# Performance work log

Hardware: AMD Instinct MI355X
Metric: run time of the kernel (lower is better)

## Reference

```python
import jax, jax.numpy as jnp
import numpy as np

CODEBOOK_SIZE = 1024
CODE_DIM = 64
COMMITMENT_COST = 0.25
EMA_DECAY = 0.99
EPS = 1e-05


def setup_inputs() -> dict:
    key = jax.random.key(0)
    k1, k2, k3, k4 = jax.random.split(key, 4)
    z = jax.random.normal(k1, (16, 4096, CODE_DIM), dtype=jnp.float32)
    codebook = jax.random.normal(k2, (CODEBOOK_SIZE, CODE_DIM), dtype=jnp.float32)
    ema_cluster_size = jax.random.uniform(k3, (CODEBOOK_SIZE,), dtype=jnp.float32)
    ema_w = jax.random.normal(k4, (CODEBOOK_SIZE, CODE_DIM), dtype=jnp.float32)
    return {"z": z, "codebook": codebook, "ema_cluster_size": ema_cluster_size, "ema_w": ema_w}


def reference(z, codebook, ema_cluster_size, ema_w):
    B, T, D = z.shape
    K = CODEBOOK_SIZE
    z_flat = z.reshape(-1, D)  # [N, D]

    # Squared-distance expansion: ||z||^2 + ||c||^2 - 2 z c^T  -> [N, K]
    distances = (
        jnp.sum(z_flat * z_flat, axis=-1, keepdims=True)
        + jnp.sum(codebook * codebook, axis=-1)
        - 2.0 * jnp.matmul(z_flat, codebook.T)
    )
    indices = jnp.argmin(distances, axis=-1)  # [N]
    z_q = codebook[indices]  # [N, D] (gathered from OLD codebook)

    # --- EMA codebook update (training, no_grad in torch) ---
    ones = jnp.ones((z_flat.shape[0],), dtype=z_flat.dtype)
    cluster_size = jax.ops.segment_sum(ones, indices, num_segments=K)  # == one_hot.sum(0)
    cluster_sum = jax.ops.segment_sum(z_flat, indices, num_segments=K)  # == one_hot.T @ z_flat
    new_ecs = ema_cluster_size * EMA_DECAY + (1.0 - EMA_DECAY) * cluster_size
    new_ew = ema_w * EMA_DECAY + (1.0 - EMA_DECAY) * cluster_sum
    n = jnp.sum(new_ecs)
    cluster_size_stable = (new_ecs + EPS) / (n + K * EPS) * n
    new_codebook = new_ew / cluster_size_stable[:, None]

    # Commitment loss (EMA path): commitment_cost * mse(z_flat, stop_grad(z_q))
    commitment_loss = jnp.mean((z_flat - jax.lax.stop_gradient(z_q)) ** 2)
    vq_loss = COMMITMENT_COST * commitment_loss

    # Straight-through estimator
    z_q_st = z_flat + jax.lax.stop_gradient(z_q - z_flat)

    z_q_out = z_q_st.reshape(B, T, D)
    indices_out = indices.reshape(B, T)
    return (z_q_out, vq_loss, indices_out, new_codebook, new_ecs, new_ew)
```

## Files before the change

kernel.cpp:

```cpp
#include <hip/hip_runtime.h>

#define KC   1024
#define DD   64
#define NR   65536

#define DECAY     0.99f
#define ONEM      0.01f
#define EPSV      1e-5f
#define MARGIN_W  0.008f

#define OFF_ZQ    0
#define OFF_LOSS  4194304
#define OFF_IDX   4194305
#define OFF_NCB   4259841
#define OFF_NECS  4325377
#define OFF_NEW   4326401


typedef float  f32x4   __attribute__((ext_vector_type(4)));
typedef short  bf16x8  __attribute__((ext_vector_type(8)));

__device__ __forceinline__ unsigned short b16(float v) {
    union { float f; unsigned u; } x; x.f = v;
    return (unsigned short)((x.u + 0x7fffu + ((x.u >> 16) & 1u)) >> 16);
}
__device__ __forceinline__ float b2f(unsigned short h) {
    union { unsigned u; float f; } x; x.u = (unsigned)h << 16;
    return x.f;
}

__device__ __forceinline__ void gload_lds16(const void* g, void* l) {
    __builtin_amdgcn_global_load_lds(
        (const __attribute__((address_space(1))) unsigned int*)g,
        (__attribute__((address_space(3))) unsigned int*)l, 16, 0, 0);
}

__global__ void vq_prep(const float* __restrict__ cb, float* __restrict__ out,
                        unsigned short* __restrict__ cbh,
                        unsigned short* __restrict__ cbm,
                        float* __restrict__ cbT) {
    const int tid = blockIdx.x * blockDim.x + threadIdx.x;
    if (tid < 65536) {
        const int code = tid >> 6, d = tid & 63;
        const int h2   = code >> 9;
        const int loc  = code & 511;
        const int ch   = loc >> 5;
        const int gloc = loc & 31;
        const int grp  = gloc >> 4;
        const int col  = gloc & 15;
        const int kh   = d >> 5;
        const int hi2  = (d >> 3) & 3;
        const int e    = d & 7;
        const int pi   = ch * 4096 + h2 * 2048 + (grp * 2 + kh) * 512
                       + (hi2 * 16 + col) * 8 + e;
        const float v = cb[tid];
        const unsigned short h = b16(v);
        cbh[pi] = h;
        cbm[pi] = b16(v - b2f(h));
        cbT[d * 1024 + code] = v;
    }
    if (tid < 1024) {
        const float4* c = reinterpret_cast<const float4*>(cb + tid * 64);
        float s = 0.f;
        #pragma unroll
        for (int j = 0; j < 16; ++j) {
            const float4 v = c[j];
            s += v.x*v.x + v.y*v.y + v.z*v.z + v.w*v.w;
        }
        out[OFF_NCB + tid] = s;
    }
    if (tid == 0) out[OFF_LOSS] = 0.0f;
}

__global__ __launch_bounds__(512, 2) void vq_main(const float* __restrict__ z,
                                                  const float* __restrict__ cc,
                                                  const unsigned short* __restrict__ cbh,
                                                  const unsigned short* __restrict__ cbm,
                                                  const float* __restrict__ cbT,
                                                  const float* __restrict__ cb,
                                                  unsigned short* __restrict__ idxw,
                                                  float* __restrict__ out) {
    const int t    = threadIdx.x;
    const int lane = t & 63;
    const int wid  = t >> 6;
    const int rowgrp = wid & 3;
    const int hf     = wid >> 2;
    const int rowbase = blockIdx.x * 128;

    __shared__ char  ldsB[4][16384];
    __shared__ float s_cc[1024];
    __shared__ float s_hd[2][128];
    __shared__ int   s_hi[2][128];
    __shared__ float s_h2[2][128];
    __shared__ int   s_final[128];
    __shared__ int   s_flag[128];
    __shared__ float s_cd[8][32];
    __shared__ int   s_cix[8][32];
    __shared__ float s_red[8];
    __shared__ int   s_nflag;

    if (t == 0) s_nflag = 0;
    s_cc[t]       = cc[t];
    s_cc[t + 512] = cc[t + 512];

    #pragma unroll
    for (int c0 = 0; c0 < 2; ++c0) {
        const char* sh = (const char*)cbh + c0 * 8192 + wid * 1024 + lane * 16;
        const char* sm = (const char*)cbm + c0 * 8192 + wid * 1024 + lane * 16;
        gload_lds16(sh, &ldsB[c0][wid * 1024]);
        gload_lds16(sm, &ldsB[c0][8192 + wid * 1024]);
    }

    bf16x8 a0h[2], a0m[2], a1h[2], a1m[2];
    #pragma unroll
    for (int tile = 0; tile < 2; ++tile) {
        const int ar = rowbase + rowgrp * 32 + tile * 16 + (lane & 15);
        const int kb = (lane >> 4) * 8;
        const float* zr = z + (size_t)ar * 64 + kb;
        const float4 v0a = *reinterpret_cast<const float4*>(zr);
        const float4 v0b = *reinterpret_cast<const float4*>(zr + 4);
        const float4 v1a = *reinterpret_cast<const float4*>(zr + 32);
        const float4 v1b = *reinterpret_cast<const float4*>(zr + 36);
        const float z0[8] = {v0a.x, v0a.y, v0a.z, v0a.w, v0b.x, v0b.y, v0b.z, v0b.w};
        const float z1[8] = {v1a.x, v1a.y, v1a.z, v1a.w, v1b.x, v1b.y, v1b.z, v1b.w};
        #pragma unroll
        for (int e = 0; e < 8; ++e) {
            const unsigned short h0 = b16(z0[e]);
            a0h[tile][e] = (short)h0;
            a0m[tile][e] = (short)b16(z0[e] - b2f(h0));
            const unsigned short h1 = b16(z1[e]);
            a1h[tile][e] = (short)h1;
            a1m[tile][e] = (short)b16(z1[e] - b2f(h1));
        }
    }
    asm volatile("s_waitcnt vmcnt(2)" ::: "memory");
    __builtin_amdgcn_s_barrier();
    __builtin_amdgcn_sched_barrier(0);

    const int lcol   = lane & 15;
    const int lane16 = lane * 16;

    float bd[2][4], b2v[2][4]; int bk[2][4];
    #pragma unroll
    for (int tile = 0; tile < 2; ++tile)
        #pragma unroll
        for (int j = 0; j < 4; ++j) {
            bd[tile][j] = 3.4e38f; b2v[tile][j] = 3.4e38f; bk[tile][j] = 0;
        }

    for (int c = 0; c < 16; ++c) {
        if (c + 2 < 16) {
            const char* sh = (const char*)cbh + (c + 2) * 8192 + wid * 1024 + lane * 16;
            const char* sm = (const char*)cbm + (c + 2) * 8192 + wid * 1024 + lane * 16;
            gload_lds16(sh, &ldsB[(c + 2) & 3][wid * 1024]);
            gload_lds16(sm, &ldsB[(c + 2) & 3][8192 + wid * 1024]);
        }
        const char* bhp = ldsB[c & 3] + hf * 4096;
        const char* bmp = ldsB[c & 3] + 8192 + hf * 4096;

        f32x4 acc00 = {0.f,0.f,0.f,0.f}, acc01 = {0.f,0.f,0.f,0.f};
        f32x4 acc10 = {0.f,0.f,0.f,0.f}, acc11 = {0.f,0.f,0.f,0.f};
        #pragma unroll
        for (int grp = 0; grp < 2; ++grp) {
            #pragma unroll
            for (int kh = 0; kh < 2; ++kh) {
                const bf16x8 bh = *reinterpret_cast<const bf16x8*>(
                    bhp + (grp * 2 + kh) * 1024 + lane16);
                const bf16x8 bm = *reinterpret_cast<const bf16x8*>(
                    bmp + (grp * 2 + kh) * 1024 + lane16);
                const bf16x8 ahh0 = kh ? a1h[0] : a0h[0];
                const bf16x8 amm0 = kh ? a1m[0] : a0m[0];
                const bf16x8 ahh1 = kh ? a1h[1] : a0h[1];
                const bf16x8 amm1 = kh ? a1m[1] : a0m[1];
                f32x4& a0 = grp ? acc01 : acc00;
                f32x4& a1 = grp ? acc11 : acc10;
                a0 = __builtin_amdgcn_mfma_f32_16x16x32_bf16(amm0, bh, a0, 0, 0, 0);
                a1 = __builtin_amdgcn_mfma_f32_16x16x32_bf16(amm1, bh, a1, 0, 0, 0);
                a0 = __builtin_amdgcn_mfma_f32_16x16x32_bf16(ahh0, bm, a0, 0, 0, 0);
                a1 = __builtin_amdgcn_mfma_f32_16x16x32_bf16(ahh1, bm, a1, 0, 0, 0);
                a0 = __builtin_amdgcn_mfma_f32_16x16x32_bf16(ahh0, bh, a0, 0, 0, 0);
                a1 = __builtin_amdgcn_mfma_f32_16x16x32_bf16(ahh1, bh, a1, 0, 0, 0);
            }
        }
        #pragma unroll
        for (int grp = 0; grp < 2; ++grp) {
            const int  code = hf * 512 + c * 32 + grp * 16 + lcol;
            const float ccv = s_cc[code];
            const f32x4 p0 = grp ? acc01 : acc00;
            const f32x4 p1 = grp ? acc11 : acc10;
            #pragma unroll
            for (int j = 0; j < 4; ++j) {
                const float s0 = fmaf(-2.f, p0[j], ccv);
                b2v[0][j] = __builtin_amdgcn_fmed3f(bd[0][j], s0, b2v[0][j]);
                if (s0 < bd[0][j]) { bd[0][j] = s0; bk[0][j] = code; }
                const float s1 = fmaf(-2.f, p1[j], ccv);
                b2v[1][j] = __builtin_amdgcn_fmed3f(bd[1][j], s1, b2v[1][j]);
                if (s1 < bd[1][j]) { bd[1][j] = s1; bk[1][j] = code; }
            }
        }

        if (c < 15) {
            if (c == 14) asm volatile("s_waitcnt vmcnt(0)" ::: "memory");
            else         asm volatile("s_waitcnt vmcnt(2)" ::: "memory");
            __builtin_amdgcn_s_barrier();
            __builtin_amdgcn_sched_barrier(0);
        }
    }

    #pragma unroll
    for (int m = 1; m < 16; m <<= 1) {
        #pragma unroll
        for (int tile = 0; tile < 2; ++tile)
            #pragma unroll
            for (int j = 0; j < 4; ++j) {
                const float od = __shfl_xor(bd[tile][j],  m);
                const int   oi = __shfl_xor(bk[tile][j],  m);
                const float o2 = __shfl_xor(b2v[tile][j], m);
                const float nb2 = fminf(fmaxf(bd[tile][j], od), fminf(b2v[tile][j], o2));
                if (od < bd[tile][j] || (od == bd[tile][j] && oi < bk[tile][j])) {
                    bd[tile][j] = od; bk[tile][j] = oi;
                }
                b2v[tile][j] = nb2;
            }
    }
    if ((lane & 15) == 0) {
        #pragma unroll
        for (int tile = 0; tile < 2; ++tile)
            #pragma unroll
            for (int j = 0; j < 4; ++j) {
                const int r = rowgrp * 32 + tile * 16 + ((lane >> 4) << 2) + j;
                s_hd[hf][r] = bd[tile][j];
                s_hi[hf][r] = bk[tile][j];
                s_h2[hf][r] = b2v[tile][j];
            }
    }
    __syncthreads();

    if (t < 128) {
        const float d0 = s_hd[0][t], d1 = s_hd[1][t];
        float bb = d0; int bi = s_hi[0][t];
        if (d1 < bb) { bb = d1; bi = s_hi[1][t]; }
        const float sec = fminf(fmaxf(d0, d1), fminf(s_h2[0][t], s_h2[1][t]));
        s_final[t] = bi;
        if (sec - bb < MARGIN_W) {
            const int p = atomicAdd(&s_nflag, 1);
            s_flag[p] = t;
        }
    }
    __syncthreads();

    const int nf = s_nflag;
    for (int fb = 0; fb < nf; fb += 32) {
        const int ne = (nf - fb < 32) ? (nf - fb) : 32;
        {
            const int cbase2 = wid * 128;
            const int c0i = cbase2 + lane, c1i = c0i + 64;
            for (int i = 0; i < ne; ++i) {
                const int r = s_flag[fb + i];
                const float* zrow = z + (size_t)(rowbase + r) * 64;
                float a0 = 0.f, a1 = 0.f;
                #pragma unroll 8
                for (int d = 0; d < 64; ++d) {
                    const float zd = zrow[d];
                    const float* cr = cbT + d * 1024 + cbase2 + lane;
                    a0 = fmaf(zd, cr[0],  a0);
                    a1 = fmaf(zd, cr[64], a1);
                }
                float bd_ = fmaf(-2.f, a0, s_cc[c0i]); int bi_ = c0i;
                const float d1 = fmaf(-2.f, a1, s_cc[c1i]);
                if (d1 < bd_) { bd_ = d1; bi_ = c1i; }
                #pragma unroll
                for (int m = 32; m >= 1; m >>= 1) {
                    const float od = __shfl_xor(bd_, m);
                    const int   oi = __shfl_xor(bi_, m);
                    if (od < bd_ || (od == bd_ && oi < bi_)) { bd_ = od; bi_ = oi; }
                }
                if (lane == 0) { s_cd[wid][i] = bd_; s_cix[wid][i] = bi_; }
            }
        }
        __syncthreads();
        if (t < ne) {
            float bd_ = s_cd[0][t]; int bi_ = s_cix[0][t];
            #pragma unroll
            for (int w = 1; w < 8; ++w) {
                const float d = s_cd[w][t]; const int i2 = s_cix[w][t];
                if (d < bd_ || (d == bd_ && i2 < bi_)) { bd_ = d; bi_ = i2; }
            }
            s_final[s_flag[fb + t]] = bi_;
        }
        __syncthreads();
    }

    if (t < 128) {
        const int k2 = s_final[t];
        out[OFF_IDX + rowbase + t] = (float)k2;
        idxw[rowbase + t] = (unsigned short)k2;
    }

    float sse = 0.f;
    const float4* zb4 = reinterpret_cast<const float4*>(z) + (size_t)blockIdx.x * 2048;
    float4*       qb  = reinterpret_cast<float4*>(out + OFF_ZQ) + (size_t)blockIdx.x * 2048;
    const float4* cb4 = reinterpret_cast<const float4*>(cb);
    #pragma unroll
    for (int j = 0; j < 4; ++j) {
        const int f  = t + 512 * j;
        const int r  = f >> 4;
        const int fc = f & 15;
        const int gk = s_final[r];
        const float4 zv = zb4[f];
        const float4 cv = cb4[gk * 16 + fc];
        qb[f] = cv;
        const float e0 = zv.x - cv.x, e1 = zv.y - cv.y;
        const float e2 = zv.z - cv.z, e3 = zv.w - cv.w;
        sse += e0 * e0 + e1 * e1 + e2 * e2 + e3 * e3;
    }

    #pragma unroll
    for (int m = 32; m >= 1; m >>= 1) sse += __shfl_xor(sse, m);
    if (lane == 0) s_red[wid] = sse;
    __syncthreads();
    if (t == 0) {
        float tot = s_red[0];
        #pragma unroll
        for (int i = 1; i < 8; ++i) tot += s_red[i];
        atomicAdd(&out[OFF_LOSS], tot);
    }
}

__global__ __launch_bounds__(512) void vq_sums(const float* __restrict__ z,
                                               const unsigned short* __restrict__ idxw,
                                               float* __restrict__ psum,
                                               float* __restrict__ pcnt) {
    const int t    = threadIdx.x;
    const int lane = t & 63;
    const int w    = t >> 6;
    const int k    = blockIdx.x >> 2;
    const int qf   = blockIdx.x & 3;
    const int base = qf * 16384 + w * 2048;

    float acc = 0.f;
    int   c   = 0;

    typedef unsigned short u16x4 __attribute__((ext_vector_type(4)));
    const u16x4* ip = reinterpret_cast<const u16x4*>(idxw + base);
    u16x4 cur = ip[lane];
    for (int s = 0; s < 8; ++s) {
        u16x4 nxt = cur;
        if (s < 7) nxt = ip[(s + 1) * 64 + lane];
        const int r0 = base + s * 256;
        c += (cur[0] == k) + (cur[1] == k) + (cur[2] == k) + (cur[3] == k);
        unsigned long long m;
        m = __ballot(cur[0] == k);
        while (m) { const int j = __ffsll((long long)m) - 1; m &= m - 1;
                    acc += z[(size_t)(r0 + 4 * j + 0) * 64 + lane]; }
        m = __ballot(cur[1] == k);
        while (m) { const int j = __ffsll((long long)m) - 1; m &= m - 1;
                    acc += z[(size_t)(r0 + 4 * j + 1) * 64 + lane]; }
        m = __ballot(cur[2] == k);
        while (m) { const int j = __ffsll((long long)m) - 1; m &= m - 1;
                    acc += z[(size_t)(r0 + 4 * j + 2) * 64 + lane]; }
        m = __ballot(cur[3] == k);
        while (m) { const int j = __ffsll((long long)m) - 1; m &= m - 1;
                    acc += z[(size_t)(r0 + 4 * j + 3) * 64 + lane]; }
        cur = nxt;
    }

    #pragma unroll
    for (int m2 = 32; m2 >= 1; m2 >>= 1) c += __shfl_xor(c, m2);

    __shared__ float s_a[8][64];
    __shared__ int   s_c[8];
    if (lane == 0) s_c[w] = c;
    s_a[w][lane] = acc;
    __syncthreads();
    if (w == 0) {
        float s = s_a[0][lane];
        #pragma unroll
        for (int i = 1; i < 8; ++i) s += s_a[i][lane];
        psum[(size_t)qf * 65536 + k * 64 + lane] = s;
        if (lane == 0) {
            int ct = s_c[0];
            #pragma unroll
            for (int i = 1; i < 8; ++i) ct += s_c[i];
            pcnt[qf * 1024 + k] = (float)ct;
        }
    }
}

__global__ __launch_bounds__(1024) void vq_final(const float* __restrict__ ema_cs,
                                                 const float* __restrict__ ema_w,
                                                 const float* __restrict__ pcnt,
                                                 const float* __restrict__ psum,
                                                 float* __restrict__ out) {
    const int k = threadIdx.x;
    const int b = blockIdx.x;
    const float cnt = ((pcnt[k] + pcnt[1024 + k]) + pcnt[2048 + k]) + pcnt[3072 + k];
    const float necs = DECAY * ema_cs[k] + ONEM * cnt;

    __shared__ float s_red[1024];
    __shared__ float s_den[1024];
    s_red[k] = necs;
    __syncthreads();
    for (int off = 512; off > 0; off >>= 1) {
        if (k < off) s_red[k] += s_red[k + off];
        __syncthreads();
    }
    const float n = s_red[0];
    s_den[k] = (necs + EPSV) / (n + (float)KC * EPSV) * n;
    if (k >= b * 16 && k < (b + 1) * 16) out[OFF_NECS + k] = necs;
    __syncthreads();

    const int e = b * 1024 + k;
    const float s = ((psum[e] + psum[65536 + e]) + psum[131072 + e]) + psum[196608 + e];
    const float ew = DECAY * ema_w[e] + ONEM * s;
    out[OFF_NEW + e] = ew;
    out[OFF_NCB + e] = ew / s_den[e >> 6];
    if (b == 0 && k == 0) out[OFF_LOSS] = 0.25f * out[OFF_LOSS] * (1.f / 4194304.f);
}

extern "C" void kernel_launch(void* const* d_in, const int* in_sizes, int n_in,
                              void* d_out, int out_size, void* d_ws, size_t ws_size,
                              hipStream_t stream) {
    const float* z   = (const float*)d_in[0];
    const float* cb  = (const float*)d_in[1];
    const float* ecs = (const float*)d_in[2];
    const float* ew  = (const float*)d_in[3];
    float* out = (float*)d_out;

    unsigned short* cbh  = (unsigned short*)d_ws;
    unsigned short* cbm  = (unsigned short*)((char*)d_ws + 131072);
    float*          cbT  = (float*)((char*)d_ws + 262144);
    unsigned short* idxw = (unsigned short*)((char*)d_ws + 524288);
    float*          pcnt = (float*)((char*)d_ws + 655360);
    float*          psum = (float*)((char*)d_ws + 671744);

    vq_prep <<<256,  256, 0, stream>>>(cb, out, cbh, cbm, cbT);
    vq_main <<<512,  512, 0, stream>>>(z, out + OFF_NCB, cbh, cbm, cbT, cb, idxw, out);
    vq_sums <<<4096, 512, 0, stream>>>(z, idxw, psum, pcnt);
    vq_final<<<64,  1024, 0, stream>>>(ecs, ew, pcnt, psum, out);
}
```

Measured before the change: 81.98 us.

## Give each wave a private double-buffered codebook stream to drop block barriers

Re-lays out the bf16 hi/lo codebook so each half of the codebook is contiguous in 16-code chunks, and gives every wave its own 8 KB LDS double buffer that it fills with direct global-to-LDS loads. The per-chunk block-wide barriers go away; each wave waits only on its own vmcnt, reads the chunk, computes the distances, then refills that slot. This removes inter-wave synchronisation stalls. In exchange every wave loads the codebook redundantly (four waves share each half), which raises global/L2 traffic, and each iteration is smaller with less MFMA work between waits.

```diff
diff --git a/kernel.cpp b/kernel.cpp
--- a/kernel.cpp
+++ b/kernel.cpp
@@ -42,17 +42,14 @@
     const int tid = blockIdx.x * blockDim.x + threadIdx.x;
     if (tid < 65536) {
         const int code = tid >> 6, d = tid & 63;
-        const int h2   = code >> 9;
+        const int hf   = code >> 9;
         const int loc  = code & 511;
-        const int ch   = loc >> 5;
-        const int gloc = loc & 31;
-        const int grp  = gloc >> 4;
-        const int col  = gloc & 15;
+        const int ch   = loc >> 4;
+        const int col  = loc & 15;
         const int kh   = d >> 5;
         const int hi2  = (d >> 3) & 3;
         const int e    = d & 7;
-        const int pi   = ch * 4096 + h2 * 2048 + (grp * 2 + kh) * 512
-                       + (hi2 * 16 + col) * 8 + e;
+        const int pi   = ((hf * 32 + ch) * 2 + kh) * 512 + (hi2 * 16 + col) * 8 + e;
         const float v = cb[tid];
         const unsigned short h = b16(v);
         cbh[pi] = h;
@@ -87,7 +84,7 @@
     const int hf     = wid >> 2;
     const int rowbase = blockIdx.x * 128;
 
-    __shared__ char  ldsB[4][16384];
+    __shared__ char  ldsB[8][8192];
     __shared__ float s_cc[1024];
     __shared__ float s_hd[2][128];
     __shared__ int   s_hi[2][128];
@@ -103,13 +100,19 @@
     s_cc[t]       = cc[t];
     s_cc[t + 512] = cc[t + 512];
 
+    char* myl = ldsB[wid];
+    const char* srcH = (const char*)cbh + (size_t)(hf * 32) * 2048;
+    const char* srcM = (const char*)cbm + (size_t)(hf * 32) * 2048;
+
     #pragma unroll
     for (int c0 = 0; c0 < 2; ++c0) {
-        const char* sh = (const char*)cbh + c0 * 8192 + wid * 1024 + lane * 16;
-        const char* sm = (const char*)cbm + c0 * 8192 + wid * 1024 + lane * 16;
-        gload_lds16(sh, &ldsB[c0][wid * 1024]);
-        gload_lds16(sm, &ldsB[c0][8192 + wid * 1024]);
-    }
+        char* dst = myl + c0 * 4096;
+        gload_lds16(srcH + c0 * 2048 +        lane * 16, dst);
+        gload_lds16(srcH + c0 * 2048 + 1024 + lane * 16, dst + 1024);
+        gload_lds16(srcM + c0 * 2048 +        lane * 16, dst + 2048);
+        gload_lds16(srcM + c0 * 2048 + 1024 + lane * 16, dst + 3072);
+    }
+    __builtin_amdgcn_sched_barrier(0);
 
     bf16x8 a0h[2], a0m[2], a1h[2], a1m[2];
     #pragma unroll
@@ -133,9 +136,7 @@
             a1m[tile][e] = (short)b16(z1[e] - b2f(h1));
         }
     }
-    asm volatile("s_waitcnt vmcnt(2)" ::: "memory");
-    __builtin_amdgcn_s_barrier();
-    __builtin_amdgcn_sched_barrier(0);
+    __syncthreads();
 
     const int lcol   = lane & 15;
     const int lane16 = lane * 16;
@@ -148,63 +149,53 @@
             bd[tile][j] = 3.4e38f; b2v[tile][j] = 3.4e38f; bk[tile][j] = 0;
         }
 
-    for (int c = 0; c < 16; ++c) {
-        if (c + 2 < 16) {
-            const char* sh = (const char*)cbh + (c + 2) * 8192 + wid * 1024 + lane * 16;
-            const char* sm = (const char*)cbm + (c + 2) * 8192 + wid * 1024 + lane * 16;
-            gload_lds16(sh, &ldsB[(c + 2) & 3][wid * 1024]);
-            gload_lds16(sm, &ldsB[(c + 2) & 3][8192 + wid * 1024]);
-        }
-        const char* bhp = ldsB[c & 3] + hf * 4096;
-        const char* bmp = ldsB[c & 3] + 8192 + hf * 4096;
-
-        f32x4 acc00 = {0.f,0.f,0.f,0.f}, acc01 = {0.f,0.f,0.f,0.f};
-        f32x4 acc10 = {0.f,0.f,0.f,0.f}, acc11 = {0.f,0.f,0.f,0.f};
-        #pragma unroll
-        for (int grp = 0; grp < 2; ++grp) {
-            #pragma unroll
-            for (int kh = 0; kh < 2; ++kh) {
-                const bf16x8 bh = *reinterpret_cast<const bf16x8*>(
-                    bhp + (grp * 2 + kh) * 1024 + lane16);
-                const bf16x8 bm = *reinterpret_cast<const bf16x8*>(
-                    bmp + (grp * 2 + kh) * 1024 + lane16);
-                const bf16x8 ahh0 = kh ? a1h[0] : a0h[0];
-                const bf16x8 amm0 = kh ? a1m[0] : a0m[0];
-                const bf16x8 ahh1 = kh ? a1h[1] : a0h[1];
-                const bf16x8 amm1 = kh ? a1m[1] : a0m[1];
-                f32x4& a0 = grp ? acc01 : acc00;
-                f32x4& a1 = grp ? acc11 : acc10;
-                a0 = __builtin_amdgcn_mfma_f32_16x16x32_bf16(amm0, bh, a0, 0, 0, 0);
-                a1 = __builtin_amdgcn_mfma_f32_16x16x32_bf16(amm1, bh, a1, 0, 0, 0);
-                a0 = __builtin_amdgcn_mfma_f32_16x16x32_bf16(ahh0, bm, a0, 0, 0, 0);
-                a1 = __builtin_amdgcn_mfma_f32_16x16x32_bf16(ahh1, bm, a1, 0, 0, 0);
-                a0 = __builtin_amdgcn_mfma_f32_16x16x32_bf16(ahh0, bh, a0, 0, 0, 0);
-                a1 = __builtin_amdgcn_mfma_f32_16x16x32_bf16(ahh1, bh, a1, 0, 0, 0);
-            }
-        }
-        #pragma unroll
-        for (int grp = 0; grp < 2; ++grp) {
-            const int  code = hf * 512 + c * 32 + grp * 16 + lcol;
-            const float ccv = s_cc[code];
-            const f32x4 p0 = grp ? acc01 : acc00;
-            const f32x4 p1 = grp ? acc11 : acc10;
-            #pragma unroll
-            for (int j = 0; j < 4; ++j) {
-                const float s0 = fmaf(-2.f, p0[j], ccv);
-                b2v[0][j] = __builtin_amdgcn_fmed3f(bd[0][j], s0, b2v[0][j]);
-                if (s0 < bd[0][j]) { bd[0][j] = s0; bk[0][j] = code; }
-                const float s1 = fmaf(-2.f, p1[j], ccv);
-                b2v[1][j] = __builtin_amdgcn_fmed3f(bd[1][j], s1, b2v[1][j]);
-                if (s1 < bd[1][j]) { bd[1][j] = s1; bk[1][j] = code; }
-            }
-        }
-
-        if (c < 15) {
-            if (c == 14) asm volatile("s_waitcnt vmcnt(0)" ::: "memory");
-            else         asm volatile("s_waitcnt vmcnt(2)" ::: "memory");
-            __builtin_amdgcn_s_barrier();
-            __builtin_amdgcn_sched_barrier(0);
-        }
+    for (int c = 0; c < 32; ++c) {
+        if (c == 31) asm volatile("s_waitcnt vmcnt(0)" ::: "memory");
+        else         asm volatile("s_waitcnt vmcnt(4)" ::: "memory");
+        __builtin_amdgcn_sched_barrier(0);
+
+        const char* bp = myl + (c & 1) * 4096;
+        const bf16x8 bh0 = *reinterpret_cast<const bf16x8*>(bp +        lane16);
+        const bf16x8 bh1 = *reinterpret_cast<const bf16x8*>(bp + 1024 + lane16);
+        const bf16x8 bm0 = *reinterpret_cast<const bf16x8*>(bp + 2048 + lane16);
+        const bf16x8 bm1 = *reinterpret_cast<const bf16x8*>(bp + 3072 + lane16);
+
+        f32x4 p0 = {0.f,0.f,0.f,0.f};
+        f32x4 p1 = {0.f,0.f,0.f,0.f};
+        p0 = __builtin_amdgcn_mfma_f32_16x16x32_bf16(a0m[0], bh0, p0, 0, 0, 0);
+        p1 = __builtin_amdgcn_mfma_f32_16x16x32_bf16(a0m[1], bh0, p1, 0, 0, 0);
+        p0 = __builtin_amdgcn_mfma_f32_16x16x32_bf16(a0h[0], bm0, p0, 0, 0, 0);
+        p1 = __builtin_amdgcn_mfma_f32_16x16x32_bf16(a0h[1], bm0, p1, 0, 0, 0);
+        p0 = __builtin_amdgcn_mfma_f32_16x16x32_bf16(a0h[0], bh0, p0, 0, 0, 0);
+        p1 = __builtin_amdgcn_mfma_f32_16x16x32_bf16(a0h[1], bh0, p1, 0, 0, 0);
+        p0 = __builtin_amdgcn_mfma_f32_16x16x32_bf16(a1m[0], bh1, p0, 0, 0, 0);
+        p1 = __builtin_amdgcn_mfma_f32_16x16x32_bf16(a1m[1], bh1, p1, 0, 0, 0);
+        p0 = __builtin_amdgcn_mfma_f32_16x16x32_bf16(a1h[0], bm1, p0, 0, 0, 0);
+        p1 = __builtin_amdgcn_mfma_f32_16x16x32_bf16(a1h[1], bm1, p1, 0, 0, 0);
+        p0 = __builtin_amdgcn_mfma_f32_16x16x32_bf16(a1h[0], bh1, p0, 0, 0, 0);
+        p1 = __builtin_amdgcn_mfma_f32_16x16x32_bf16(a1h[1], bh1, p1, 0, 0, 0);
+
+        const int  code = hf * 512 + c * 16 + lcol;
+        const float ccv = s_cc[code];
+        #pragma unroll
+        for (int j = 0; j < 4; ++j) {
+            const float s0 = fmaf(-2.f, p0[j], ccv);
+            b2v[0][j] = __builtin_amdgcn_fmed3f(bd[0][j], s0, b2v[0][j]);
+            if (s0 < bd[0][j]) { bd[0][j] = s0; bk[0][j] = code; }
+            const float s1 = fmaf(-2.f, p1[j], ccv);
+            b2v[1][j] = __builtin_amdgcn_fmed3f(bd[1][j], s1, b2v[1][j]);
+            if (s1 < bd[1][j]) { bd[1][j] = s1; bk[1][j] = code; }
+        }
+
+        __builtin_amdgcn_sched_barrier(0);
+        if (c + 2 < 32) {
+            char* dst = myl + (c & 1) * 4096;
+            gload_lds16(srcH + (c + 2) * 2048 +        lane * 16, dst);
+            gload_lds16(srcH + (c + 2) * 2048 + 1024 + lane * 16, dst + 1024);
+            gload_lds16(srcM + (c + 2) * 2048 +        lane * 16, dst + 2048);
+            gload_lds16(srcM + (c + 2) * 2048 + 1024 + lane * 16, dst + 3072);
+        }
+        __builtin_amdgcn_sched_barrier(0);
     }
 
     #pragma unroll
```

Measured after the change: 84.40 us. 3.0% more time.
